# Kernel optimization log

Measured on AMD Instinct MI355X. Metric: run time of the kernel, lower is better.

The kernel has to match this reference:

```python
import jax, jax.numpy as jnp
import numpy as np

EPS = 1e-6


def _safe_norm(x, axis, keepdims=True):
    # sqrt with zero-safe gradient (double-where trick)
    sq = (x * x).sum(axis=axis, keepdims=keepdims)
    safe = jnp.where(sq > 0, sq, 1.0)
    return jnp.where(sq > 0, jnp.sqrt(safe), 0.0)


def _complex_coord_norm(lig, pro, lig_mask, pro_mask, set_weights):
    # 'length' norm over the joint complex: scale each set so the mean vector
    # length over all real (lig + pro) nodes is ~1, with a learnable per-set weight.
    lig_len = _safe_norm(lig, axis=-1, keepdims=False) * lig_mask   # [B,S,Nl]
    pro_len = _safe_norm(pro, axis=-1, keepdims=False) * pro_mask   # [B,S,Np]
    total_len = lig_len.sum(-1) + pro_len.sum(-1)                   # [B,S]
    n_atoms = lig_mask.sum(-1) + pro_mask.sum(-1)                   # [B,S]
    mean_len = (total_len / n_atoms)[..., None, None]               # [B,S,1,1]
    w = set_weights[None, :, None, None]
    lig = lig * w / (mean_len + EPS) * lig_mask[..., None]
    pro = pro * w / (mean_len + EPS) * pro_mask[..., None]
    return lig, pro


def setup_inputs() -> dict:
    key = jax.random.key(0)
    ks = jax.random.split(key, 8)
    B, S, P, Nl, Np = 8, 64, 64, 128, 256
    scale = 1.0 / np.sqrt(S)
    return {
        "lig_coord_sets": jax.random.normal(ks[0], (B, S, Nl, 3), jnp.float32),
        "messages": jax.random.normal(ks[1], (B, Nl, Nl + Np, P), jnp.float32),
        "adj_matrix": jax.random.randint(ks[2], (B, Nl, Nl + Np), 0, 2, jnp.int32),
        "lig_node_mask": jnp.ones((B, S, Nl), jnp.float32),
        "pro_coord_sets": jax.random.normal(ks[3], (B, S, Np, 3), jnp.float32),
        "pro_node_mask": jnp.ones((B, S, Np), jnp.float32),
        "lig_proj_w": jax.random.normal(ks[4], (P, S), jnp.float32) * scale,
        "pro_proj_w": jax.random.normal(ks[5], (P, S), jnp.float32) * scale,
        "attn_proj_w": jax.random.normal(ks[6], (S, P), jnp.float32) * scale,
        "set_weights": jnp.ones((S,), jnp.float32),
    }


def reference(lig_coord_sets, messages, adj_matrix, lig_node_mask,
              pro_coord_sets, pro_node_mask,
              lig_proj_w, pro_proj_w, attn_proj_w, set_weights):
    B, S, Nl, _ = lig_coord_sets.shape
    lig, pro = _complex_coord_norm(lig_coord_sets, pro_coord_sets,
                                   lig_node_mask, pro_node_mask, set_weights)
    # Linear over the sets dim: [B,S,N,3] -> [B,3,N,P]
    lig_p = jnp.einsum('bsnc,ps->bcnp', lig, lig_proj_w)
    pro_p = jnp.einsum('bsnc,ps->bcnp', pro, pro_proj_w)
    proj = jnp.concatenate([lig_p, pro_p], axis=2)        # [B,3,N,P]
    # pairwise vector diffs, ligand queries only (matches post-hoc slice in torch)
    vec = proj[:, :, :Nl, None, :] - proj[:, :, None, :, :]   # [B,3,Nl,N,P]
    lengths = _safe_norm(vec, axis=1)                          # [B,1,Nl,N,P]
    norm_dists = vec / (lengths + EPS)
    attn_mask = jnp.where(adj_matrix > 0, 0.0, -jnp.inf)       # [B,Nl,N]
    attn = jax.nn.softmax(messages + attn_mask[..., None], axis=2)  # [B,Nl,N,P]
    upd = jnp.einsum('bcinp,binp->bcip', norm_dists, attn)     # [B,3,Nl,P]
    weights = jnp.sqrt((attn * attn).sum(axis=2))              # [B,Nl,P]
    upd = upd * weights[:, None]
    # attn_proj (P -> S) + transpose(1,-1): [B,3,Nl,P] -> [B,S,Nl,3]
    return jnp.einsum('bcip,sp->bsic', upd, attn_proj_w)
```

## Files before the change

### kernel.cpp

```cpp
#include <hip/hip_runtime.h>
#include <hip/hip_bf16.h>
#include <math.h>

#define B   8
#define S   64
#define NL  128
#define NPRO 256
#define NN  384
#define P   64
#define NGRP 8
#define EPSF 1e-6f

__global__ __launch_bounds__(64) void meanlen_kernel(
    const float* __restrict__ lig, const float* __restrict__ ligmask,
    const float* __restrict__ pro, const float* __restrict__ promask,
    float* __restrict__ meanlen)
{
    int blk = blockIdx.x;
    int t = threadIdx.x;
    float suml = 0.f, cnt = 0.f;

    const float* lbase = lig + (size_t)blk * NL * 3;
    const float* lm    = ligmask + (size_t)blk * NL;
    for (int n = t; n < NL; n += 64) {
        float x = lbase[n*3+0], y = lbase[n*3+1], z = lbase[n*3+2];
        float mk = lm[n];
        suml += sqrtf(x*x + y*y + z*z) * mk;
        cnt  += mk;
    }
    const float* pbase = pro + (size_t)blk * NPRO * 3;
    const float* pm    = promask + (size_t)blk * NPRO;
    for (int n = t; n < NPRO; n += 64) {
        float x = pbase[n*3+0], y = pbase[n*3+1], z = pbase[n*3+2];
        float mk = pm[n];
        suml += sqrtf(x*x + y*y + z*z) * mk;
        cnt  += mk;
    }
    for (int off = 32; off > 0; off >>= 1) {
        suml += __shfl_down(suml, off);
        cnt  += __shfl_down(cnt,  off);
    }
    if (t == 0) meanlen[blk] = suml / cnt;
}

__global__ __launch_bounds__(64) void proj_kernel(
    const float* __restrict__ lig, const float* __restrict__ pro,
    const float* __restrict__ ligmask, const float* __restrict__ promask,
    const float* __restrict__ ligw, const float* __restrict__ prow,
    const float* __restrict__ sw, const float* __restrict__ meanlen,
    float4* __restrict__ proj4)
{
    int blk = blockIdx.x;
    int b = blk / (NN / NGRP);
    int g = blk - b * (NN / NGRP);
    int nbase = g * NGRP;
    int t = threadIdx.x;
    bool isl = (nbase < NL);

    __shared__ float wl[64][65];
    const float* w = isl ? ligw : prow;
    for (int row = 0; row < 64; ++row) wl[row][t] = w[row * 64 + t];

    __shared__ float cs[NGRP][3][64];
    {
        int s = t;
        float gfac = sw[s] / (meanlen[b * S + s] + EPSF);
        for (int nn = 0; nn < NGRP; ++nn) {
            int n = nbase + nn;
            float mk, X, Y, Z;
            if (isl) {
                size_t base = ((size_t)b * S + s) * NL + n;
                mk = ligmask[base];
                X = lig[base*3+0]; Y = lig[base*3+1]; Z = lig[base*3+2];
            } else {
                size_t base = ((size_t)b * S + s) * NPRO + (n - NL);
                mk = promask[base];
                X = pro[base*3+0]; Y = pro[base*3+1]; Z = pro[base*3+2];
            }
            float gg = gfac * mk;
            cs[nn][0][s] = X * gg;
            cs[nn][1][s] = Y * gg;
            cs[nn][2][s] = Z * gg;
        }
    }
    __syncthreads();

    for (int nn = 0; nn < NGRP; ++nn) {
        float a0 = 0.f, a1 = 0.f, a2 = 0.f;
        #pragma unroll 8
        for (int s = 0; s < 64; ++s) {
            float wv = wl[t][s];
            a0 += cs[nn][0][s] * wv;
            a1 += cs[nn][1][s] * wv;
            a2 += cs[nn][2][s] * wv;
        }
        proj4[((size_t)b * NN + nbase + nn) * P + t] = make_float4(a0, a1, a2, 0.f);
    }
}

__global__ __launch_bounds__(512) void attn_kernel(
    const float* __restrict__ messages,
    const int*   __restrict__ adj,
    const float4* __restrict__ proj4,
    const float* __restrict__ attn_w,
    float* __restrict__ out)
{
    int blk = blockIdx.x;
    int b = blk >> 7;
    int i = blk & (NL - 1);
    int t = threadIdx.x;
    int p = t & 63;
    int slice = t >> 6;

    __shared__ float amask[NN];
    __shared__ float wt[64][64];
    __shared__ float ls1[8][64], ls2[8][64];
    __shared__ float la0[8][64], la1[8][64], la2[8][64];
    __shared__ float upd[3][64];

    const int* adj_base = adj + (size_t)blk * NN;
    for (int n = t; n < NN; n += 512)
        amask[n] = adj_base[n] > 0 ? 0.f : -INFINITY;
    for (int idx = t; idx < 64 * 64; idx += 512) {
        int s = idx >> 6, pp = idx & 63;
        wt[pp][s] = attn_w[idx];
    }

    float4 xi = proj4[((size_t)b * NN + i) * P + p];
    const float* msg_base = messages + (size_t)blk * NN * P;
    const float4* pb = proj4 + (size_t)b * NN * P;

    __syncthreads();

    float s1 = 0.f, s2 = 0.f;
    float a0 = 0.f, a1 = 0.f, a2 = 0.f;

    int n0 = slice * (NN / 8);
    #pragma unroll 8
    for (int k = 0; k < NN / 8; ++k) {
        int n = n0 + k;
        float msg = msg_base[(size_t)n * P + p];
        float4 xn = pb[(size_t)n * P + p];

        float x = msg + amask[n];

        float d0 = xi.x - xn.x, d1 = xi.y - xn.y, d2 = xi.z - xn.z;
        float sq = fmaf(d0, d0, fmaf(d1, d1, d2 * d2));
        float inv;
        asm("v_rsq_f32 %0, %1" : "=v"(inv) : "v"(sq));
        inv = sq > 0.f ? inv : 0.f;

        float e  = __expf(x);
        float ei = e * inv;
        s1 += e;
        s2 = fmaf(e, e, s2);
        a0 = fmaf(ei, d0, a0);
        a1 = fmaf(ei, d1, a1);
        a2 = fmaf(ei, d2, a2);
    }

    ls1[slice][p] = s1; ls2[slice][p] = s2;
    la0[slice][p] = a0; la1[slice][p] = a1; la2[slice][p] = a2;
    __syncthreads();

    if (t < 64) {
        float S1 = 0.f, S2 = 0.f, A0 = 0.f, A1 = 0.f, A2 = 0.f;
        #pragma unroll
        for (int k = 0; k < 8; ++k) {
            S1 += ls1[k][p];
            S2 += ls2[k][p];
            A0 += la0[k][p];
            A1 += la1[k][p];
            A2 += la2[k][p];
        }
        float wgt = sqrtf(S2) / (S1 * S1);
        upd[0][p] = A0 * wgt;
        upd[1][p] = A1 * wgt;
        upd[2][p] = A2 * wgt;
    }
    __syncthreads();

    if (t < 192) {
        int s = t & 63, c = t >> 6;
        float o = 0.f;
        #pragma unroll 8
        for (int pp = 0; pp < P; ++pp)
            o = fmaf(upd[c][pp], wt[pp][s], o);
        out[(((size_t)b * S + s) * NL + i) * 3 + c] = o;
    }
}

extern "C" void kernel_launch(void* const* d_in, const int* in_sizes, int n_in,
                              void* d_out, int out_size, void* d_ws, size_t ws_size,
                              hipStream_t stream)
{
    const float* lig      = (const float*)d_in[0];
    const float* messages = (const float*)d_in[1];
    const int*   adj      = (const int*)  d_in[2];
    const float* ligmask  = (const float*)d_in[3];
    const float* pro      = (const float*)d_in[4];
    const float* promask  = (const float*)d_in[5];
    const float* ligw     = (const float*)d_in[6];
    const float* prow     = (const float*)d_in[7];
    const float* attnw    = (const float*)d_in[8];
    const float* sw       = (const float*)d_in[9];
    float* out = (float*)d_out;

    float*  meanlen = (float*)d_ws;
    float4* proj4   = (float4*)((char*)d_ws + 2048);

    meanlen_kernel<<<B * S, 64, 0, stream>>>(lig, ligmask, pro, promask, meanlen);
    proj_kernel<<<B * (NN / NGRP), 64, 0, stream>>>(lig, pro, ligmask, promask,
                                                    ligw, prow, sw, meanlen, proj4);
    attn_kernel<<<B * NL, 512, 0, stream>>>(messages, adj, proj4, attnw, out);
}
```

Baseline: 52.33 us.

## Split projection into SoA planes and vectorize attention loop with float4 loads

The padded float4 AoS projection buffer becomes three separate x/y/z planes, so the attention kernel no longer reads a wasted fourth component. Each thread now handles four P channels through float4 loads over a 12-node slice, with a manual one-step prefetch and native exp2/rsq instructions. Partial sums are reduced within the wave by xor shuffles before going to shared memory. The attn_w LDS staging is dropped in favour of direct float4 global reads. This raises register pressure and puts more work on the shuffle reduction in exchange for wider, less wasteful memory access.

Result: slower. 53.80 us (+2.8%).

```diff
diff --git a/kernel.cpp b/kernel.cpp
--- a/kernel.cpp
+++ b/kernel.cpp
@@ -48,7 +48,7 @@
     const float* __restrict__ ligmask, const float* __restrict__ promask,
     const float* __restrict__ ligw, const float* __restrict__ prow,
     const float* __restrict__ sw, const float* __restrict__ meanlen,
-    float4* __restrict__ proj4)
+    float* __restrict__ projx, float* __restrict__ projy, float* __restrict__ projz)
 {
     int blk = blockIdx.x;
     int b = blk / (NN / NGRP);
@@ -94,14 +94,35 @@
             a1 += cs[nn][1][s] * wv;
             a2 += cs[nn][2][s] * wv;
         }
-        proj4[((size_t)b * NN + nbase + nn) * P + t] = make_float4(a0, a1, a2, 0.f);
-    }
-}
+        size_t base = ((size_t)b * NN + nbase + nn) * P;
+        projx[base + t] = a0;
+        projy[base + t] = a1;
+        projz[base + t] = a2;
+    }
+}
+
+#define PROC(C) { \
+    float d0 = xix.C - xx.C, d1 = xiy.C - yy.C, d2 = xiz.C - zz.C; \
+    float sq = fmaf(d0, d0, fmaf(d1, d1, d2 * d2)); \
+    float inv; asm("v_rsq_f32 %0, %1" : "=v"(inv) : "v"(sq)); \
+    inv = sq > 0.f ? inv : 0.f; \
+    float xe = fmaf(mm.C, 1.44269504f, am); \
+    float e; asm("v_exp_f32 %0, %1" : "=v"(e) : "v"(xe)); \
+    S1.C += e; S2.C = fmaf(e, e, S2.C); \
+    float ei = e * inv; \
+    A0.C = fmaf(ei, d0, A0.C); \
+    A1.C = fmaf(ei, d1, A1.C); \
+    A2.C = fmaf(ei, d2, A2.C); }
+
+#define RED(V) { V.x += __shfl_xor(V.x, off); V.y += __shfl_xor(V.y, off); \
+                 V.z += __shfl_xor(V.z, off); V.w += __shfl_xor(V.w, off); }
 
 __global__ __launch_bounds__(512) void attn_kernel(
     const float* __restrict__ messages,
     const int*   __restrict__ adj,
-    const float4* __restrict__ proj4,
+    const float* __restrict__ projx,
+    const float* __restrict__ projy,
+    const float* __restrict__ projz,
     const float* __restrict__ attn_w,
     float* __restrict__ out)
 {
@@ -109,11 +130,13 @@
     int b = blk >> 7;
     int i = blk & (NL - 1);
     int t = threadIdx.x;
-    int p = t & 63;
-    int slice = t >> 6;
+    int lane = t & 63;
+    int wave = t >> 6;
+    int pg = lane & 15;
+    int wsl = lane >> 4;
+    int slice = wave * 4 + wsl;
 
     __shared__ float amask[NN];
-    __shared__ float wt[64][64];
     __shared__ float ls1[8][64], ls2[8][64];
     __shared__ float la0[8][64], la1[8][64], la2[8][64];
     __shared__ float upd[3][64];
@@ -121,71 +144,78 @@
     const int* adj_base = adj + (size_t)blk * NN;
     for (int n = t; n < NN; n += 512)
         amask[n] = adj_base[n] > 0 ? 0.f : -INFINITY;
-    for (int idx = t; idx < 64 * 64; idx += 512) {
-        int s = idx >> 6, pp = idx & 63;
-        wt[pp][s] = attn_w[idx];
-    }
-
-    float4 xi = proj4[((size_t)b * NN + i) * P + p];
-    const float* msg_base = messages + (size_t)blk * NN * P;
-    const float4* pb = proj4 + (size_t)b * NN * P;
-
-    __syncthreads();
-
-    float s1 = 0.f, s2 = 0.f;
-    float a0 = 0.f, a1 = 0.f, a2 = 0.f;
-
-    int n0 = slice * (NN / 8);
-    #pragma unroll 8
-    for (int k = 0; k < NN / 8; ++k) {
-        int n = n0 + k;
-        float msg = msg_base[(size_t)n * P + p];
-        float4 xn = pb[(size_t)n * P + p];
-
-        float x = msg + amask[n];
-
-        float d0 = xi.x - xn.x, d1 = xi.y - xn.y, d2 = xi.z - xn.z;
-        float sq = fmaf(d0, d0, fmaf(d1, d1, d2 * d2));
-        float inv;
-        asm("v_rsq_f32 %0, %1" : "=v"(inv) : "v"(sq));
-        inv = sq > 0.f ? inv : 0.f;
-
-        float e  = __expf(x);
-        float ei = e * inv;
-        s1 += e;
-        s2 = fmaf(e, e, s2);
-        a0 = fmaf(ei, d0, a0);
-        a1 = fmaf(ei, d1, a1);
-        a2 = fmaf(ei, d2, a2);
-    }
-
-    ls1[slice][p] = s1; ls2[slice][p] = s2;
-    la0[slice][p] = a0; la1[slice][p] = a1; la2[slice][p] = a2;
+
+    const float4* m4  = (const float4*)messages + (size_t)blk * NN * 16;
+    const float4* px4 = (const float4*)projx + (size_t)b * NN * 16;
+    const float4* py4 = (const float4*)projy + (size_t)b * NN * 16;
+    const float4* pz4 = (const float4*)projz + (size_t)b * NN * 16;
+
+    float4 xix = px4[(size_t)i * 16 + pg];
+    float4 xiy = py4[(size_t)i * 16 + pg];
+    float4 xiz = pz4[(size_t)i * 16 + pg];
+
+    __syncthreads();
+
+    float4 S1 = {0,0,0,0}, S2 = {0,0,0,0};
+    float4 A0 = {0,0,0,0}, A1 = {0,0,0,0}, A2 = {0,0,0,0};
+
+    int nb = slice * 12;
+    size_t idx0 = (size_t)nb * 16 + pg;
+    float4 mc = m4[idx0], xc = px4[idx0], yc = py4[idx0], zc = pz4[idx0];
+
+    #pragma unroll
+    for (int k = 0; k < 12; ++k) {
+        int n = nb + k;
+        float4 mm = mc, xx = xc, yy = yc, zz = zc;
+        if (k < 11) {
+            size_t idx = (size_t)(n + 1) * 16 + pg;
+            mc = m4[idx]; xc = px4[idx]; yc = py4[idx]; zc = pz4[idx];
+        }
+        float am = amask[n];
+        PROC(x) PROC(y) PROC(z) PROC(w)
+    }
+
+    #pragma unroll
+    for (int off = 16; off <= 32; off <<= 1) {
+        RED(S1) RED(S2) RED(A0) RED(A1) RED(A2)
+    }
+
+    if (wsl == 0) {
+        int pbase = pg * 4;
+        ls1[wave][pbase+0] = S1.x; ls1[wave][pbase+1] = S1.y; ls1[wave][pbase+2] = S1.z; ls1[wave][pbase+3] = S1.w;
+        ls2[wave][pbase+0] = S2.x; ls2[wave][pbase+1] = S2.y; ls2[wave][pbase+2] = S2.z; ls2[wave][pbase+3] = S2.w;
+        la0[wave][pbase+0] = A0.x; la0[wave][pbase+1] = A0.y; la0[wave][pbase+2] = A0.z; la0[wave][pbase+3] = A0.w;
+        la1[wave][pbase+0] = A1.x; la1[wave][pbase+1] = A1.y; la1[wave][pbase+2] = A1.z; la1[wave][pbase+3] = A1.w;
+        la2[wave][pbase+0] = A2.x; la2[wave][pbase+1] = A2.y; la2[wave][pbase+2] = A2.z; la2[wave][pbase+3] = A2.w;
+    }
     __syncthreads();
 
     if (t < 64) {
-        float S1 = 0.f, S2 = 0.f, A0 = 0.f, A1 = 0.f, A2 = 0.f;
+        float s1 = 0.f, s2 = 0.f, a0 = 0.f, a1 = 0.f, a2 = 0.f;
         #pragma unroll
-        for (int k = 0; k < 8; ++k) {
-            S1 += ls1[k][p];
-            S2 += ls2[k][p];
-            A0 += la0[k][p];
-            A1 += la1[k][p];
-            A2 += la2[k][p];
-        }
-        float wgt = sqrtf(S2) / (S1 * S1);
-        upd[0][p] = A0 * wgt;
-        upd[1][p] = A1 * wgt;
-        upd[2][p] = A2 * wgt;
+        for (int w = 0; w < 8; ++w) {
+            s1 += ls1[w][t]; s2 += ls2[w][t];
+            a0 += la0[w][t]; a1 += la1[w][t]; a2 += la2[w][t];
+        }
+        float wgt = sqrtf(s2) / (s1 * s1);
+        upd[0][t] = a0 * wgt;
+        upd[1][t] = a1 * wgt;
+        upd[2][t] = a2 * wgt;
     }
     __syncthreads();
 
     if (t < 192) {
         int s = t & 63, c = t >> 6;
+        const float4* aw4 = (const float4*)attn_w + (size_t)s * 16;
         float o = 0.f;
-        #pragma unroll 8
-        for (int pp = 0; pp < P; ++pp)
-            o = fmaf(upd[c][pp], wt[pp][s], o);
+        #pragma unroll
+        for (int q = 0; q < 16; ++q) {
+            float4 w4 = aw4[q];
+            o = fmaf(upd[c][q*4+0], w4.x, o);
+            o = fmaf(upd[c][q*4+1], w4.y, o);
+            o = fmaf(upd[c][q*4+2], w4.z, o);
+            o = fmaf(upd[c][q*4+3], w4.w, o);
+        }
         out[(((size_t)b * S + s) * NL + i) * 3 + c] = o;
     }
 }
@@ -206,11 +236,16 @@
     const float* sw       = (const float*)d_in[9];
     float* out = (float*)d_out;
 
-    float*  meanlen = (float*)d_ws;
-    float4* proj4   = (float4*)((char*)d_ws + 2048);
+    const size_t plane = (size_t)B * NN * P;
+    float* meanlen = (float*)d_ws;
+    float* projx   = (float*)((char*)d_ws + 2048);
+    float* projy   = projx + plane;
+    float* projz   = projy + plane;
 
     meanlen_kernel<<<B * S, 64, 0, stream>>>(lig, ligmask, pro, promask, meanlen);
     proj_kernel<<<B * (NN / NGRP), 64, 0, stream>>>(lig, pro, ligmask, promask,
-                                                    ligw, prow, sw, meanlen, proj4);
-    attn_kernel<<<B * NL, 512, 0, stream>>>(messages, adj, proj4, attnw, out);
-}
+                                                    ligw, prow, sw, meanlen,
+                                                    projx, projy, projz);
+    attn_kernel<<<B * NL, 512, 0, stream>>>(messages, adj, projx, projy, projz,
+                                            attnw, out);
+}
```
